# Optimization experiments

Measured on AMD Instinct MI355X. Metric: run time of the kernel, lower is better.

Reference implementation:

```python
import jax, jax.numpy as jnp
import numpy as np

NS, NV, NB, L = 64, 32, 8, 4      # scalar channels, vector channels, bessel bases, layers
EMB = 32                           # atom-type embedding dim
MAX_R = 3.0                        # cutoff radius
NUM_NEIGH = 32.0                   # avg degree used for scatter normalization
N, E = 10000, 320000
NW = NS * 2 + NV * 2               # per-edge tensor-product weights from radial MLP
MAX_TYPES = 10


def smooth_cutoff(x):
    # e3nn md-example smooth_cutoff: 1 for x<0.5, 0 for x>1, cosine blend between
    u = 2.0 * (x - 1.0)
    y = (1.0 - jnp.cos(jnp.pi * u)) * 0.5
    y = jnp.where(u > 0.0, 0.0, y)
    y = jnp.where(u < -1.0, 1.0, y)
    return y


def bessel_basis(r):
    # soft_one_hot_linspace(basis='bessel', cutoff=False) * sqrt(NB)
    n = jnp.arange(1, NB + 1, dtype=r.dtype)
    y = jnp.sqrt(2.0 / MAX_R) * jnp.sin(n * jnp.pi * r[:, None] / MAX_R) / r[:, None]
    return y * np.sqrt(NB).astype(np.float32)


def edge_info(x, src, dst):
    feats, attrs = [], []
    for i in range(2):  # nvec = x.shape[-1] // 3 = 2
        vec = x[src, 3 * i:3 * i + 3] - x[dst, 3 * i:3 * i + 3]  # [E,3]
        r = jnp.linalg.norm(vec, axis=1)
        sh = np.float32(np.sqrt(3.0)) * vec / r[:, None]          # 1x1o SH, component norm
        feats.append(bessel_basis(r))
        attrs.append(smooth_cutoff(r / MAX_R)[:, None] * sh)
    return jnp.concatenate(feats, axis=-1), jnp.stack(attrs, axis=1)  # [E,2*NB], [E,2,3]


def _forward(x, emb_table, W_up, W_proj, fc1, b1, fc2, W_sv, W_vs, W_sc_s, W_sc_v, Ws, Wv, h, mix, node_attr, edge_src, edge_dst):
    n = x.shape[0]
    inv_nb = np.float32(1.0 / np.sqrt(NUM_NEIGH))
    # uplift: 2 input vectors -> NV hidden vectors, NS hidden scalars (zero init)
    xv = x.reshape(n, 2, 3)
    v = jnp.einsum('nic,iv->nvc', xv, W_up)        # [n,NV,3]
    s = jnp.zeros((n, NS), x.dtype)                # [n,NS]
    s_old, v_old = s, v
    attr_emb = emb_table[node_attr]                # [n,EMB]
    xcur = x
    for i in range(L):
        f, a = edge_info(xcur, edge_src, edge_dst)            # [E,2NB], [E,2,3]
        w = jax.nn.silu(f @ fc1[i] + b1[i]) @ fc2[i]          # [E,NW] radial TP weights
        w1 = w[:, :NS * 2].reshape(-1, NS, 2)                 # 0e x 1o -> 1o path weights
        w2 = w[:, NS * 2:].reshape(-1, NV, 2)                 # 1o x 1o -> 0e path weights
        # equivariant tensor-product messages (gather at edge_src)
        t = s[edge_src][:, :, None] * w1                      # [E,NS,2]
        q = jnp.einsum('euv,uvm->evm', t, W_sv[i])            # [E,2,NV]
        msg_v = jnp.einsum('evm,evc->emc', q, a)              # [E,NV,3]
        d = jnp.einsum('euc,evc->euv', v[edge_src], a)        # [E,NV,2]
        msg_s = jnp.einsum('euv,uvm->em', d * w2, W_vs[i])    # [E,NS+NV]
        # scatter-add at edge_dst, normalized by sqrt(num_neighbors)
        agg_s = jnp.zeros((n, NS + NV), x.dtype).at[edge_dst].add(msg_s) * inv_nb
        agg_v = jnp.zeros((n, NV, 3), x.dtype).at[edge_dst].add(msg_v) * inv_nb
        # self-connection: fully-connected TP with node-attr scalars
        sc_s = jnp.einsum('nu,ne,uem->nm', s, attr_emb, W_sc_s[i])
        sc_v = jnp.einsum('nuc,ne,uev->nvc', v, attr_emb, W_sc_v[i])
        cs = sc_s + agg_s
        cv = sc_v + agg_v
        # Gate: silu on scalars, sigmoid gate scalars modulate vectors
        gs = jax.nn.silu(cs[:, :NS])
        gate = jax.nn.sigmoid(cs[:, NS:])
        gv = cv * gate[:, :, None]
        # self-interaction (equivariant linear per degree)
        si_s = s @ Ws[i]
        si_v = jnp.einsum('nuc,uv->nvc', v, Wv[i])
        # verlet-like update
        hi2 = h[i] ** 2
        s_new = 2.0 * s - s_old + hi2 * (mix[i] * gs + (mix[i] - 1.0) * si_s)
        v_new = 2.0 * v - v_old + hi2 * (mix[i] * gv + (mix[i] - 1.0) * si_v)
        s_old, v_old = s, v
        s, v = s_new, v_new
        # project back to x for next layer's edge features
        xcur = jnp.einsum('nvc,vi->nic', v, W_proj).reshape(n, 6)
    return xcur


def setup_inputs() -> dict:
    key = jax.random.key(0)
    ks = jax.random.split(key, 20)
    x = jax.random.normal(ks[0], (N, 6), jnp.float32)
    node_attr = jax.random.randint(ks[1], (N,), 0, MAX_TYPES)
    edge_src = jax.random.randint(ks[2], (E,), 0, N)
    off = jax.random.randint(ks[3], (E,), 1, N)
    edge_dst = (edge_src + off) % N  # no self-loops -> no zero edge_vec
    batch = jnp.zeros((N,), jnp.int32)
    rn = lambda k, sh, sc: jax.random.normal(k, sh, jnp.float32) * np.float32(sc)
    emb_table = rn(ks[4], (MAX_TYPES, EMB), 0.5)
    W_up = rn(ks[5], (2, NV), 1.0 / np.sqrt(2))
    W_proj = rn(ks[6], (NV, 2), 1.0 / np.sqrt(NV))
    fc1 = rn(ks[7], (L, 2 * NB, 64), 1.0 / np.sqrt(2 * NB))
    b1 = jnp.zeros((L, 64), jnp.float32)
    fc2 = rn(ks[8], (L, 64, NW), 1.0 / np.sqrt(64))
    W_sv = rn(ks[9], (L, NS, 2, NV), 1.0 / np.sqrt(NS * 2))
    W_vs = rn(ks[10], (L, NV, 2, NS + NV), 1.0 / np.sqrt(NV * 2))
    W_sc_s = rn(ks[11], (L, NS, EMB, NS + NV), 1.0 / np.sqrt(NS * EMB))
    W_sc_v = rn(ks[12], (L, NV, EMB, NV), 1.0 / np.sqrt(NV * EMB))
    Ws = rn(ks[13], (L, NS, NS), 1.0 / np.sqrt(NS))
    Wv = rn(ks[14], (L, NV, NV), 1.0 / np.sqrt(NV))
    h = jnp.ones((L,), jnp.float32) * 0.01
    mix = jnp.ones((L,), jnp.float32) * 0.5
    return {"x": x, "emb_table": emb_table, "W_up": W_up, "W_proj": W_proj, "fc1": fc1, "b1": b1, "fc2": fc2, "W_sv": W_sv, "W_vs": W_vs, "W_sc_s": W_sc_s, "W_sc_v": W_sc_v, "Ws": Ws, "Wv": Wv, "h": h, "mix": mix, "node_attr": node_attr, "edge_src": edge_src, "edge_dst": edge_dst, "batch": batch}


def reference(x, emb_table, W_up, W_proj, fc1, b1, fc2, W_sv, W_vs, W_sc_s, W_sc_v, Ws, Wv, h, mix, node_attr, edge_src, edge_dst, batch):
    return _forward(x, emb_table, W_up, W_proj, fc1, b1, fc2, W_sv, W_vs, W_sc_s, W_sc_v, Ws, Wv, h, mix, node_attr, edge_src, edge_dst)
```

## Files before the change

kernel.cpp:

```cpp
#include <hip/hip_runtime.h>
#include <math.h>

constexpr int cNS = 64, cNV = 32, cNB = 8, cL = 4, cEMB = 32, cNT = 10;
constexpr float PI_F = 3.14159265358979323846f;
constexpr float INV_SQRT_NN = 0.17677669529663687f;
constexpr float BESSEL_C = 2.3094010767585034f;
constexpr float SQRT3 = 1.7320508075688772f;

typedef unsigned short u16;
typedef unsigned int u32;
typedef __attribute__((ext_vector_type(8))) short bf16x8;
typedef __attribute__((ext_vector_type(4))) float f32x4;
typedef __attribute__((ext_vector_type(2))) float f32x2;
typedef __attribute__((ext_vector_type(4))) int i32x4;

__device__ __forceinline__ u16 f2b(float x) {
  u32 u = __float_as_uint(x);
  return (u16)((u + 0x7fffu + ((u >> 16) & 1u)) >> 16);
}
__device__ __forceinline__ float b2f(u16 h) { return __uint_as_float(((u32)h) << 16); }

__device__ __forceinline__ f32x4 mfma16(bf16x8 a, bf16x8 b, f32x4 c) {
  return __builtin_amdgcn_mfma_f32_16x16x32_bf16(a, b, c, 0, 0, 0);
}


__global__ void k_precompA(const float* __restrict__ emb, const float* __restrict__ Wss,
                           float* __restrict__ A) {
  int idx = blockIdx.x * 256 + threadIdx.x;
  if (idx >= cL * cNT * 64 * 96) return;
  int m = idx % 96;
  int u = (idx / 96) % 64;
  int t = (idx / (96 * 64)) % cNT;
  int l = idx / (96 * 64 * cNT);
  float acc = 0.f;
#pragma unroll
  for (int e = 0; e < 32; ++e)
    acc += emb[t * 32 + e] * Wss[((size_t)(l * 64 + u) * 32 + e) * 96 + m];
  A[idx] = acc;
}

__global__ void k_precompB(const float* __restrict__ emb, const float* __restrict__ Wsv_,
                           float* __restrict__ B) {
  int idx = blockIdx.x * 256 + threadIdx.x;
  if (idx >= cL * cNT * 32 * 32) return;
  int vo = idx % 32;
  int u = (idx / 32) % 32;
  int t = (idx / 1024) % cNT;
  int l = idx / (1024 * cNT);
  float acc = 0.f;
#pragma unroll
  for (int e = 0; e < 32; ++e)
    acc += emb[t * 32 + e] * Wsv_[((size_t)(l * 32 + u) * 32 + e) * 32 + vo];
  B[idx] = acc;
}

__global__ void k_packB(const float* __restrict__ fc2, const float* __restrict__ Wsv,
                        const float* __restrict__ Wvs, const float* __restrict__ fc1,
                        u16* __restrict__ fc2L, u16* __restrict__ WsvL,
                        u16* __restrict__ WvsL, u16* __restrict__ fc1L) {
  int idx = blockIdx.x * 256 + threadIdx.x;
  const int T1 = cL * 12288, T2 = cL * 2 * 2048, T3 = cL * 2 * 3072, T4 = cL * 2048;
  if (idx < T1) {
    int l = idx / 12288, r = idx % 12288;
    int ki = r & 7, tt = r >> 3;
    int nn = tt % 192, kq = tt / 192;
    fc2L[idx] = f2b(fc2[((size_t)(l * 64) + kq * 8 + ki) * 192 + nn]);
  } else if (idx < T1 + T2) {
    int r0 = idx - T1;
    int l = r0 / 4096, r1 = r0 % 4096;
    int k2 = r1 / 2048, r = r1 % 2048;
    int ki = r & 7, tt = r >> 3;
    int mm = tt % 32, kq = tt / 32;
    WsvL[r0] = f2b(Wsv[((size_t)((l * 64 + kq * 8 + ki) * 2) + k2) * 32 + mm]);
  } else if (idx < T1 + T2 + T3) {
    int r0 = idx - T1 - T2;
    int l = r0 / 6144, r1 = r0 % 6144;
    int k2 = r1 / 3072, r = r1 % 3072;
    int ki = r & 7, tt = r >> 3;
    int mm = tt % 96, kq = tt / 96;
    WvsL[r0] = f2b(Wvs[((size_t)((l * 32 + kq * 8 + ki) * 2) + k2) * 96 + mm]);
  } else if (idx < T1 + T2 + T3 + T4) {
    int r0 = idx - T1 - T2 - T3;
    int l = r0 / 2048, r1 = r0 % 2048;
    int kq = r1 / 512, rem = r1 % 512;
    int n = rem / 8, ki = rem & 7;
    fc1L[r0] = (kq < 2) ? f2b(fc1[l * 1024 + (kq * 8 + ki) * 64 + n]) : (u16)0;
  }
}

__global__ void k_init(const float* __restrict__ x, const float* __restrict__ Wup,
                       float* __restrict__ v, float* __restrict__ v_old,
                       float* __restrict__ xcur, int N) {
  int idx = blockIdx.x * 256 + threadIdx.x;
  if (idx >= N * 32) return;
  int n = idx >> 5, vc = idx & 31;
  float w0 = Wup[vc], w1 = Wup[32 + vc];
#pragma unroll
  for (int c = 0; c < 3; ++c) {
    float val = x[n * 6 + c] * w0 + x[n * 6 + 3 + c] * w1;
    v[idx * 3 + c] = val;
    v_old[idx * 3 + c] = val;
  }
  if (vc < 6) xcur[n * 6 + vc] = x[n * 6 + vc];
}


__global__ void k_zero_i(int* __restrict__ p, int n) {
  int i = blockIdx.x * 256 + threadIdx.x;
  if (i < n) p[i] = 0;
}

__global__ void k_hist(const int* __restrict__ edst, int* __restrict__ deg, int E) {
  int e = blockIdx.x * 256 + threadIdx.x;
  if (e < E) atomicAdd(&deg[edst[e]], 1);
}

__global__ __launch_bounds__(1024) void k_scan(const int* __restrict__ deg,
                                               int* __restrict__ row_ptr,
                                               int* __restrict__ cursor, int N) {
  __shared__ int part[1024];
  int t = threadIdx.x;
  int chunk = (N + 1023) / 1024;
  int base = t * chunk;
  int sum = 0;
  for (int i = 0; i < chunk; ++i) {
    int idx = base + i;
    if (idx < N) sum += deg[idx];
  }
  part[t] = sum;
  __syncthreads();
  for (int off = 1; off < 1024; off <<= 1) {
    int val = (t >= off) ? part[t - off] : 0;
    __syncthreads();
    part[t] += val;
    __syncthreads();
  }
  int run = (t > 0) ? part[t - 1] : 0;
  for (int i = 0; i < chunk; ++i) {
    int idx = base + i;
    if (idx < N) {
      row_ptr[idx] = run;
      cursor[idx] = run;
      run += deg[idx];
    }
  }
  if (t == 1023) row_ptr[N] = part[1023];
}

__global__ void k_scatter(const int* __restrict__ esrc, const int* __restrict__ edst,
                          int* __restrict__ cursor, int* __restrict__ esrc_s,
                          int* __restrict__ edst_s, int E) {
  int e = blockIdx.x * 256 + threadIdx.x;
  if (e < E) {
    int d = edst[e];
    int p = atomicAdd(&cursor[d], 1);
    esrc_s[p] = esrc[e];
    edst_s[p] = d;
  }
}

template <bool SZERO>
__global__ __launch_bounds__(256) void k_edge_mfma(
    const float* __restrict__ xcur, const float* __restrict__ s, const float* __restrict__ v,
    const int* __restrict__ esrc_s, const int* __restrict__ edst_s,
    const u16* __restrict__ fc1L, const float* __restrict__ b1,
    const u16* __restrict__ fc2L, const u16* __restrict__ WsvL0,
    const u16* __restrict__ WsvL1, const u16* __restrict__ WvsL0,
    const u16* __restrict__ WvsL1, u16* __restrict__ msgbuf, int E) {
  __shared__ u16 wbAll[4][16 * 200];
  __shared__ float aAll[4][16][6];
  int wid = threadIdx.x >> 6, lane = threadIdx.x & 63;
  int e0 = (blockIdx.x * 4 + wid) * 16;
  if (e0 >= E) return;
  u16* wb = wbAll[wid];
  int lrow = lane & 15, lg = lane >> 4;

  {
    int el = lane >> 2, qq = lane & 3;
    int ge = e0 + el;
    if (ge >= E) ge = E - 1;
    int gs = esrc_s[ge], gd = edst_s[ge];
    float xs[6], xd[6];
    {
      const float2* ps = (const float2*)(xcur + (size_t)gs * 6);
      const float2* pd = (const float2*)(xcur + (size_t)gd * 6);
      float2 A0 = ps[0], A1 = ps[1], A2 = ps[2];
      float2 B0 = pd[0], B1 = pd[1], B2 = pd[2];
      xs[0] = A0.x; xs[1] = A0.y; xs[2] = A1.x; xs[3] = A1.y; xs[4] = A2.x; xs[5] = A2.y;
      xd[0] = B0.x; xd[1] = B0.y; xd[2] = B1.x; xd[3] = B1.y; xd[4] = B2.x; xd[5] = B2.y;
    }
    float f[16], av[6];
#pragma unroll
    for (int i = 0; i < 2; ++i) {
      float vx = xs[3 * i + 0] - xd[3 * i + 0];
      float vy = xs[3 * i + 1] - xd[3 * i + 1];
      float vz = xs[3 * i + 2] - xd[3 * i + 2];
      float r2 = vx * vx + vy * vy + vz * vz;
      float rr = sqrtf(r2);
      float invr = 1.0f / rr;
      float th = (PI_F / 3.0f) * rr;
      float s1, c1;
      __sincosf(th, &s1, &c1);
      float twc = 2.0f * c1;
      float snm = 0.f, sn = s1;
      float fc = BESSEL_C * invr;
#pragma unroll
      for (int nn = 0; nn < 8; ++nn) {
        f[8 * i + nn] = fc * sn;
        float nx = twc * sn - snm;
        snm = sn;
        sn = nx;
      }
      float uu = (2.0f / 3.0f) * rr - 2.0f;
      float cut;
      if (uu > 0.f) cut = 0.f;
      else if (uu < -1.f) cut = 1.f;
      else cut = (1.0f - __cosf(PI_F * uu)) * 0.5f;
      float sc = cut * SQRT3 * invr;
      av[3 * i + 0] = vx * sc; av[3 * i + 1] = vy * sc; av[3 * i + 2] = vz * sc;
    }
    if (qq == 0) {
      u32* fp = (u32*)(wb + 1600 + el * 32);
#pragma unroll
      for (int i = 0; i < 8; ++i)
        fp[i] = (u32)f2b(f[2 * i]) | ((u32)f2b(f[2 * i + 1]) << 16);
#pragma unroll
      for (int i = 8; i < 16; ++i) fp[i] = 0u;
      float* ap = aAll[wid][el];
#pragma unroll
      for (int i = 0; i < 6; ++i) ap[i] = av[i];
    }
  }
  asm volatile("s_waitcnt lgkmcnt(0)" ::: "memory");
  __builtin_amdgcn_sched_barrier(0);

  {
    bf16x8 fA = *(const bf16x8*)(wb + 1600 + lrow * 32 + lg * 8);
    f32x4 hp[4];
#pragma unroll
    for (int nb = 0; nb < 4; ++nb) {
      bf16x8 bB = *(const bf16x8*)(fc1L + (size_t)(lg * 64 + nb * 16 + lrow) * 8);
      f32x4 z = {0.f, 0.f, 0.f, 0.f};
      hp[nb] = mfma16(fA, bB, z);
    }
#pragma unroll
    for (int nb = 0; nb < 4; ++nb) {
      float bias = b1[nb * 16 + lrow];
#pragma unroll
      for (int r = 0; r < 4; ++r) {
        float xv = hp[nb][r] + bias;
        float hv = xv * (1.0f / (1.0f + __expf(-xv)));
        wb[(4 * lg + r) * 72 + nb * 16 + lrow] = f2b(hv);
      }
    }
  }
  asm volatile("s_waitcnt lgkmcnt(0)" ::: "memory");
  __builtin_amdgcn_sched_barrier(0);

  int prow = e0 + lrow;
  if (prow >= E) prow = E - 1;

  bf16x8 ha = *(const bf16x8*)(wb + lrow * 72 + lg * 8);
  bf16x8 hbf = *(const bf16x8*)(wb + lrow * 72 + 32 + lg * 8);
  asm volatile("s_waitcnt lgkmcnt(0)" ::: "memory");

#pragma unroll
  for (int nb = (SZERO ? 8 : 0); nb < 12; ++nb) {
    bf16x8 b0 = *(const bf16x8*)(fc2L + (size_t)(lg * 192 + nb * 16 + lrow) * 8);
    bf16x8 b1v = *(const bf16x8*)(fc2L + (size_t)((4 + lg) * 192 + nb * 16 + lrow) * 8);
    f32x4 c = {0.f, 0.f, 0.f, 0.f};
    c = mfma16(ha, b0, c);
    c = mfma16(hbf, b1v, c);
    int n = nb * 16 + lrow;
    int pn = (n < 128) ? ((n & 1) * 64 + (n >> 1)) : (128 + (n & 1) * 32 + ((n - 128) >> 1));
    int rbase = 4 * lg * 200 + pn;
    wb[rbase] = f2b(c[0]);
    wb[rbase + 200] = f2b(c[1]);
    wb[rbase + 400] = f2b(c[2]);
    wb[rbase + 600] = f2b(c[3]);
  }
  asm volatile("s_waitcnt lgkmcnt(0)" ::: "memory");

  int src = esrc_s[prow];
  const u16* wrow = wb + lrow * 200;

  f32x4 q0[2], q1[2];
  if (!SZERO) {
    const float* sp = s + (size_t)src * 64;
    float sv0[8], sv1[8];
    *(f32x4*)(sv0) = *(const f32x4*)(sp + lg * 8);
    *(f32x4*)(sv0 + 4) = *(const f32x4*)(sp + lg * 8 + 4);
    *(f32x4*)(sv1) = *(const f32x4*)(sp + 32 + lg * 8);
    *(f32x4*)(sv1 + 4) = *(const f32x4*)(sp + 32 + lg * 8 + 4);
    bf16x8 w0a = *(const bf16x8*)(wrow + lg * 8);
    bf16x8 w0b = *(const bf16x8*)(wrow + 32 + lg * 8);
    bf16x8 w1a = *(const bf16x8*)(wrow + 64 + lg * 8);
    bf16x8 w1b = *(const bf16x8*)(wrow + 96 + lg * 8);
    bf16x8 t0a, t0b, t1a, t1b;
#pragma unroll
    for (int j = 0; j < 8; ++j) {
      t0a[j] = (short)f2b(sv0[j] * b2f((u16)w0a[j]));
      t0b[j] = (short)f2b(sv1[j] * b2f((u16)w0b[j]));
      t1a[j] = (short)f2b(sv0[j] * b2f((u16)w1a[j]));
      t1b[j] = (short)f2b(sv1[j] * b2f((u16)w1b[j]));
    }
#pragma unroll
    for (int nb = 0; nb < 2; ++nb) {
      bf16x8 bA = *(const bf16x8*)(WsvL0 + (size_t)(lg * 32 + nb * 16 + lrow) * 8);
      bf16x8 bB = *(const bf16x8*)(WsvL0 + (size_t)((4 + lg) * 32 + nb * 16 + lrow) * 8);
      f32x4 c = {0.f, 0.f, 0.f, 0.f};
      c = mfma16(t0a, bA, c);
      c = mfma16(t0b, bB, c);
      q0[nb] = c;
      bf16x8 bC = *(const bf16x8*)(WsvL1 + (size_t)(lg * 32 + nb * 16 + lrow) * 8);
      bf16x8 bD = *(const bf16x8*)(WsvL1 + (size_t)((4 + lg) * 32 + nb * 16 + lrow) * 8);
      f32x4 c2 = {0.f, 0.f, 0.f, 0.f};
      c2 = mfma16(t1a, bC, c2);
      c2 = mfma16(t1b, bD, c2);
      q1[nb] = c2;
    }
  }

  float a00, a01, a02, a10, a11, a12;
  {
    const float* ap = aAll[wid][lrow];
    a00 = ap[0]; a01 = ap[1]; a02 = ap[2]; a10 = ap[3]; a11 = ap[4]; a12 = ap[5];
  }
  float vl[24];
  {
    const float* vp = v + (size_t)src * 96 + lg * 24;
#pragma unroll
    for (int i = 0; i < 6; ++i) *(f32x4*)(vl + 4 * i) = *(const f32x4*)(vp + 4 * i);
  }
  bf16x8 w2a = *(const bf16x8*)(wrow + 128 + lg * 8);
  bf16x8 w2b = *(const bf16x8*)(wrow + 160 + lg * 8);
  bf16x8 ga, gb;
#pragma unroll
  for (int j = 0; j < 8; ++j) {
    float vx = vl[3 * j], vy = vl[3 * j + 1], vz = vl[3 * j + 2];
    float d0 = vx * a00 + vy * a01 + vz * a02;
    float d1 = vx * a10 + vy * a11 + vz * a12;
    ga[j] = (short)f2b(d0 * b2f((u16)w2a[j]));
    gb[j] = (short)f2b(d1 * b2f((u16)w2b[j]));
  }
  f32x4 mS[6];
#pragma unroll
  for (int nb = 0; nb < 6; ++nb) {
    bf16x8 b0 = *(const bf16x8*)(WvsL0 + (size_t)(lg * 96 + nb * 16 + lrow) * 8);
    bf16x8 b1v = *(const bf16x8*)(WvsL1 + (size_t)(lg * 96 + nb * 16 + lrow) * 8);
    f32x4 c = {0.f, 0.f, 0.f, 0.f};
    c = mfma16(ga, b0, c);
    c = mfma16(gb, b1v, c);
    mS[nb] = c;
  }

  asm volatile("s_waitcnt lgkmcnt(0)" ::: "memory");
#pragma unroll
  for (int nb = 0; nb < 6; ++nb) {
#pragma unroll
    for (int r = 0; r < 4; ++r)
      wb[(4 * lg + r) * 200 + nb * 16 + lrow] = f2b(mS[nb][r]);
  }
  if (!SZERO) {
#pragma unroll
    for (int nb = 0; nb < 2; ++nb) {
#pragma unroll
      for (int r = 0; r < 4; ++r) {
        int el = 4 * lg + r;
        const float* ap = aAll[wid][el];
        float Q0v = q0[nb][r], Q1v = q1[nb][r];
#pragma unroll
        for (int c = 0; c < 3; ++c)
          wb[el * 200 + 96 + c * 32 + nb * 16 + lrow] = f2b(Q0v * ap[c] + Q1v * ap[3 + c]);
      }
    }
  }
  asm volatile("s_waitcnt lgkmcnt(0)" ::: "memory");

  int orow = lane >> 2, oq = lane & 3;
  if (e0 + orow < E) {
    u16* gdst = msgbuf + (size_t)(e0 + orow) * 192;
    const int NIT = SZERO ? 3 : 6;
#pragma unroll
    for (int it = 0; it < NIT; ++it) {
      int col = oq * 8 + it * 32;
      i32x4 d = *(const i32x4*)(wb + orow * 200 + col);
      *(i32x4*)(gdst + col) = d;
    }
  }
}

template <bool SZERO>
__global__ __launch_bounds__(128) void k_gnode(
    const u16* __restrict__ msg, const int* __restrict__ row_ptr,
    float* __restrict__ s, float* __restrict__ sold, float* __restrict__ v,
    float* __restrict__ vold,
    const float* __restrict__ Amat, const float* __restrict__ Bmat,
    const float* __restrict__ Ws, const float* __restrict__ Wv,
    const float* __restrict__ Wproj, const int* __restrict__ nattr,
    const float* __restrict__ hArr, const float* __restrict__ mixArr, int layer,
    float* __restrict__ xout, int N) {
  int n = blockIdx.x;
  int t = threadIdx.x;
  __shared__ float agg[192];
  __shared__ float srow[64];
  __shared__ float vrow[96];
  __shared__ float gateS[32];
  __shared__ float vnewS[96];
  int start = row_ptr[n], end = row_ptr[n + 1];
  int nacc = SZERO ? 48 : 96;
  if (t < nacc) {
    const u16* mp = msg + (size_t)t * 2;
    float l0 = 0.f, h0 = 0.f, l1 = 0.f, h1 = 0.f;
    float l2 = 0.f, h2 = 0.f, l3 = 0.f, h3 = 0.f;
    int p = start;
    for (; p + 4 <= end; p += 4) {
      u32 w0 = *(const u32*)(mp + (size_t)p * 192);
      u32 w1 = *(const u32*)(mp + (size_t)(p + 1) * 192);
      u32 w2 = *(const u32*)(mp + (size_t)(p + 2) * 192);
      u32 w3 = *(const u32*)(mp + (size_t)(p + 3) * 192);
      l0 += b2f((u16)w0); h0 += b2f((u16)(w0 >> 16));
      l1 += b2f((u16)w1); h1 += b2f((u16)(w1 >> 16));
      l2 += b2f((u16)w2); h2 += b2f((u16)(w2 >> 16));
      l3 += b2f((u16)w3); h3 += b2f((u16)(w3 >> 16));
    }
    for (; p < end; ++p) {
      u32 w = *(const u32*)(mp + (size_t)p * 192);
      l0 += b2f((u16)w); h0 += b2f((u16)(w >> 16));
    }
    agg[2 * t] = (l0 + l1 + l2 + l3) * INV_SQRT_NN;
    agg[2 * t + 1] = (h0 + h1 + h2 + h3) * INV_SQRT_NN;
  }
  if (SZERO && t >= 48 && t < 96) {
    agg[2 * t] = 0.f;
    agg[2 * t + 1] = 0.f;
  }
  if (t < 64) srow[t] = s[(size_t)n * 64 + t];
  if (t < 96) vrow[t] = v[(size_t)n * 96 + t];
  __syncthreads();
  int type = nattr[n];
  float hv = hArr[layer];
  float h2v = hv * hv;
  float mx = mixArr[layer];
  float cs = 0.f;
  if (t < 96) {
    cs = agg[t];
    const float* Ac = Amat + (size_t)type * 64 * 96 + t;
#pragma unroll 8
    for (int u = 0; u < 64; ++u) cs += srow[u] * Ac[u * 96];
  }
  if (t >= 64 && t < 96) gateS[t - 64] = 1.0f / (1.0f + __expf(-cs));
  __syncthreads();
  if (t < 64) {
    float gs = cs * (1.0f / (1.0f + __expf(-cs)));
    float sis = 0.f;
#pragma unroll 8
    for (int u = 0; u < 64; ++u) sis += srow[u] * Ws[u * 64 + t];
    float scur = srow[t];
    float sprev = sold[(size_t)n * 64 + t];
    float snew = 2.f * scur - sprev + h2v * (mx * gs + (mx - 1.f) * sis);
    sold[(size_t)n * 64 + t] = scur;
    s[(size_t)n * 64 + t] = snew;
  }
  if (t < 96) {
    int vch = t / 3, c = t - vch * 3;
    float cv = agg[96 + c * 32 + vch];
    const float* Bc = Bmat + (size_t)type * 1024 + vch;
    float scv = 0.f, siv = 0.f;
#pragma unroll 8
    for (int u = 0; u < 32; ++u) {
      float vu = vrow[u * 3 + c];
      scv += vu * Bc[u * 32];
      siv += vu * Wv[u * 32 + vch];
    }
    cv += scv;
    float gv = cv * gateS[vch];
    float vcur = vrow[t];
    float vprev = vold[(size_t)n * 96 + t];
    float vnew = 2.f * vcur - vprev + h2v * (mx * gv + (mx - 1.f) * siv);
    vold[(size_t)n * 96 + t] = vcur;
    v[(size_t)n * 96 + t] = vnew;
    vnewS[t] = vnew;
  }
  __syncthreads();
  if (t < 6) {
    int i = t / 3, c = t - i * 3;
    float acc = 0.f;
#pragma unroll
    for (int vo = 0; vo < 32; ++vo) acc += vnewS[vo * 3 + c] * Wproj[vo * 2 + i];
    xout[(size_t)n * 6 + t] = acc;
  }
}

extern "C" void kernel_launch(void* const* d_in, const int* in_sizes, int n_in,
                              void* d_out, int out_size, void* d_ws, size_t ws_size,
                              hipStream_t stream) {
  const float* x = (const float*)d_in[0];
  const float* emb = (const float*)d_in[1];
  const float* Wup = (const float*)d_in[2];
  const float* Wproj = (const float*)d_in[3];
  const float* fc1 = (const float*)d_in[4];
  const float* b1 = (const float*)d_in[5];
  const float* fc2 = (const float*)d_in[6];
  const float* Wsv = (const float*)d_in[7];
  const float* Wvs = (const float*)d_in[8];
  const float* Wscs = (const float*)d_in[9];
  const float* Wscv = (const float*)d_in[10];
  const float* Ws = (const float*)d_in[11];
  const float* Wv = (const float*)d_in[12];
  const float* hArr = (const float*)d_in[13];
  const float* mixArr = (const float*)d_in[14];
  const int* nattr = (const int*)d_in[15];
  const int* esrc = (const int*)d_in[16];
  const int* edst = (const int*)d_in[17];

  const int N = in_sizes[0] / 6;
  const int E = in_sizes[16];

  float* ws = (float*)d_ws;
  size_t off = 0;
  auto alloc = [&](size_t nf) {
    float* p = ws + off;
    off += (nf + 3) & ~(size_t)3;
    return p;
  };
  float* sbuf = alloc((size_t)N * 64);
  float* sold = alloc((size_t)N * 64);
  float* vbuf = alloc((size_t)N * 96);
  float* vold = alloc((size_t)N * 96);
  float* xcur = alloc((size_t)N * 6);
  float* Amat = alloc((size_t)cL * cNT * 64 * 96);
  float* Bmat = alloc((size_t)cL * cNT * 32 * 32);
  u16* fc2L = (u16*)alloc((size_t)cL * 6144);
  u16* WsvL = (u16*)alloc((size_t)cL * 2048);
  u16* WvsL = (u16*)alloc((size_t)cL * 3072);
  u16* fc1L = (u16*)alloc((size_t)cL * 1024);
  int* deg = (int*)alloc((size_t)(N + 4));
  int* row_ptr = (int*)alloc((size_t)(N + 4));
  int* cursor = (int*)alloc((size_t)(N + 4));
  int* esrc_s = (int*)alloc((size_t)E);
  int* edst_s = (int*)alloc((size_t)E);
  u16* msgbuf = (u16*)alloc((size_t)E * 96);

  hipMemsetAsync(sbuf, 0, sizeof(float) * (size_t)N * 128, stream);
  k_init<<<(N * 32 + 255) / 256, 256, 0, stream>>>(x, Wup, vbuf, vold, xcur, N);
  k_precompA<<<(cL * cNT * 64 * 96 + 255) / 256, 256, 0, stream>>>(emb, Wscs, Amat);
  k_precompB<<<(cL * cNT * 32 * 32 + 255) / 256, 256, 0, stream>>>(emb, Wscv, Bmat);
  {
    int tot = cL * 12288 + cL * 4096 + cL * 6144 + cL * 2048;
    k_packB<<<(tot + 255) / 256, 256, 0, stream>>>(fc2, Wsv, Wvs, fc1, fc2L, WsvL, WvsL, fc1L);
  }
  k_zero_i<<<(N + 255) / 256, 256, 0, stream>>>(deg, N);
  k_hist<<<(E + 255) / 256, 256, 0, stream>>>(edst, deg, E);
  k_scan<<<1, 1024, 0, stream>>>(deg, row_ptr, cursor, N);
  k_scatter<<<(E + 255) / 256, 256, 0, stream>>>(esrc, edst, cursor, esrc_s, edst_s, E);

  int eblocks = ((E + 15) / 16 + 3) / 4;
  for (int l = 0; l < cL; ++l) {
    if (l == 0)
      k_edge_mfma<true><<<eblocks, 256, 0, stream>>>(
          xcur, sbuf, vbuf, esrc_s, edst_s, fc1L + l * 2048, b1 + l * 64,
          fc2L + l * 12288, WsvL + l * 4096, WsvL + l * 4096 + 2048,
          WvsL + l * 6144, WvsL + l * 6144 + 3072, msgbuf, E);
    else
      k_edge_mfma<false><<<eblocks, 256, 0, stream>>>(
          xcur, sbuf, vbuf, esrc_s, edst_s, fc1L + l * 2048, b1 + l * 64,
          fc2L + l * 12288, WsvL + l * 4096, WsvL + l * 4096 + 2048,
          WvsL + l * 6144, WvsL + l * 6144 + 3072, msgbuf, E);
    float* xout = (l == cL - 1) ? (float*)d_out : xcur;
    if (l == 0)
      k_gnode<true><<<N, 128, 0, stream>>>(
          msgbuf, row_ptr, sbuf, sold, vbuf, vold, Amat + (size_t)l * cNT * 64 * 96,
          Bmat + (size_t)l * cNT * 1024, Ws + l * 4096, Wv + l * 1024, Wproj, nattr,
          hArr, mixArr, l, xout, N);
    else
      k_gnode<false><<<N, 128, 0, stream>>>(
          msgbuf, row_ptr, sbuf, sold, vbuf, vold, Amat + (size_t)l * cNT * 64 * 96,
          Bmat + (size_t)l * cNT * 1024, Ws + l * 4096, Wv + l * 1024, Wproj, nattr,
          hArr, mixArr, l, xout, N);
  }
}
```

Measured before the change: 558.0 us.

## Pack bf16 conversions with v_cvt_pk and compact message stride for zero-scalar layer

```diff
diff --git a/kernel.cpp b/kernel.cpp
--- a/kernel.cpp
+++ b/kernel.cpp
@@ -19,6 +19,16 @@
   return (u16)((u + 0x7fffu + ((u >> 16) & 1u)) >> 16);
 }
 __device__ __forceinline__ float b2f(u16 h) { return __uint_as_float(((u32)h) << 16); }
+__device__ __forceinline__ float blo(u32 w) { return __uint_as_float(w << 16); }
+__device__ __forceinline__ float bhi(u32 w) { return __uint_as_float(w & 0xffff0000u); }
+
+__device__ __forceinline__ u32 pkbf(float lo, float hi) {
+  u32 r;
+  asm("v_cvt_pk_bf16_f32 %0, %1, %2" : "=v"(r) : "v"(lo), "v"(hi));
+  return r;
+}
+
+union U8 { bf16x8 v; u32 w[4]; };
 
 __device__ __forceinline__ f32x4 mfma16(bf16x8 a, bf16x8 b, f32x4 c) {
   return __builtin_amdgcn_mfma_f32_16x16x32_bf16(a, b, c, 0, 0, 0);
@@ -223,8 +233,7 @@
     if (qq == 0) {
       u32* fp = (u32*)(wb + 1600 + el * 32);
 #pragma unroll
-      for (int i = 0; i < 8; ++i)
-        fp[i] = (u32)f2b(f[2 * i]) | ((u32)f2b(f[2 * i + 1]) << 16);
+      for (int i = 0; i < 8; ++i) fp[i] = pkbf(f[2 * i], f[2 * i + 1]);
 #pragma unroll
       for (int i = 8; i < 16; ++i) fp[i] = 0u;
       float* ap = aAll[wid][el];
@@ -247,12 +256,19 @@
 #pragma unroll
     for (int nb = 0; nb < 4; ++nb) {
       float bias = b1[nb * 16 + lrow];
+      float hv[4];
 #pragma unroll
       for (int r = 0; r < 4; ++r) {
         float xv = hp[nb][r] + bias;
-        float hv = xv * (1.0f / (1.0f + __expf(-xv)));
-        wb[(4 * lg + r) * 72 + nb * 16 + lrow] = f2b(hv);
+        hv[r] = xv * (1.0f / (1.0f + __expf(-xv)));
       }
+      u32 p01 = pkbf(hv[0], hv[1]);
+      u32 p23 = pkbf(hv[2], hv[3]);
+      int col = nb * 16 + lrow;
+      wb[(4 * lg + 0) * 72 + col] = (u16)p01;
+      wb[(4 * lg + 1) * 72 + col] = (u16)(p01 >> 16);
+      wb[(4 * lg + 2) * 72 + col] = (u16)p23;
+      wb[(4 * lg + 3) * 72 + col] = (u16)(p23 >> 16);
     }
   }
   asm volatile("s_waitcnt lgkmcnt(0)" ::: "memory");
@@ -275,10 +291,12 @@
     int n = nb * 16 + lrow;
     int pn = (n < 128) ? ((n & 1) * 64 + (n >> 1)) : (128 + (n & 1) * 32 + ((n - 128) >> 1));
     int rbase = 4 * lg * 200 + pn;
-    wb[rbase] = f2b(c[0]);
-    wb[rbase + 200] = f2b(c[1]);
-    wb[rbase + 400] = f2b(c[2]);
-    wb[rbase + 600] = f2b(c[3]);
+    u32 p01 = pkbf(c[0], c[1]);
+    u32 p23 = pkbf(c[2], c[3]);
+    wb[rbase] = (u16)p01;
+    wb[rbase + 200] = (u16)(p01 >> 16);
+    wb[rbase + 400] = (u16)p23;
+    wb[rbase + 600] = (u16)(p23 >> 16);
   }
   asm volatile("s_waitcnt lgkmcnt(0)" ::: "memory");
 
@@ -293,31 +311,32 @@
     *(f32x4*)(sv0 + 4) = *(const f32x4*)(sp + lg * 8 + 4);
     *(f32x4*)(sv1) = *(const f32x4*)(sp + 32 + lg * 8);
     *(f32x4*)(sv1 + 4) = *(const f32x4*)(sp + 32 + lg * 8 + 4);
-    bf16x8 w0a = *(const bf16x8*)(wrow + lg * 8);
-    bf16x8 w0b = *(const bf16x8*)(wrow + 32 + lg * 8);
-    bf16x8 w1a = *(const bf16x8*)(wrow + 64 + lg * 8);
-    bf16x8 w1b = *(const bf16x8*)(wrow + 96 + lg * 8);
-    bf16x8 t0a, t0b, t1a, t1b;
-#pragma unroll
-    for (int j = 0; j < 8; ++j) {
-      t0a[j] = (short)f2b(sv0[j] * b2f((u16)w0a[j]));
-      t0b[j] = (short)f2b(sv1[j] * b2f((u16)w0b[j]));
-      t1a[j] = (short)f2b(sv0[j] * b2f((u16)w1a[j]));
-      t1b[j] = (short)f2b(sv1[j] * b2f((u16)w1b[j]));
+    i32x4 W0a = *(const i32x4*)(wrow + lg * 8);
+    i32x4 W0b = *(const i32x4*)(wrow + 32 + lg * 8);
+    i32x4 W1a = *(const i32x4*)(wrow + 64 + lg * 8);
+    i32x4 W1b = *(const i32x4*)(wrow + 96 + lg * 8);
+    U8 t0a, t0b, t1a, t1b;
+#pragma unroll
+    for (int j2 = 0; j2 < 4; ++j2) {
+      u32 wa = (u32)W0a[j2], wbv = (u32)W0b[j2], wc = (u32)W1a[j2], wd = (u32)W1b[j2];
+      t0a.w[j2] = pkbf(sv0[2 * j2] * blo(wa), sv0[2 * j2 + 1] * bhi(wa));
+      t0b.w[j2] = pkbf(sv1[2 * j2] * blo(wbv), sv1[2 * j2 + 1] * bhi(wbv));
+      t1a.w[j2] = pkbf(sv0[2 * j2] * blo(wc), sv0[2 * j2 + 1] * bhi(wc));
+      t1b.w[j2] = pkbf(sv1[2 * j2] * blo(wd), sv1[2 * j2 + 1] * bhi(wd));
     }
 #pragma unroll
     for (int nb = 0; nb < 2; ++nb) {
       bf16x8 bA = *(const bf16x8*)(WsvL0 + (size_t)(lg * 32 + nb * 16 + lrow) * 8);
       bf16x8 bB = *(const bf16x8*)(WsvL0 + (size_t)((4 + lg) * 32 + nb * 16 + lrow) * 8);
       f32x4 c = {0.f, 0.f, 0.f, 0.f};
-      c = mfma16(t0a, bA, c);
-      c = mfma16(t0b, bB, c);
+      c = mfma16(t0a.v, bA, c);
+      c = mfma16(t0b.v, bB, c);
       q0[nb] = c;
       bf16x8 bC = *(const bf16x8*)(WsvL1 + (size_t)(lg * 32 + nb * 16 + lrow) * 8);
       bf16x8 bD = *(const bf16x8*)(WsvL1 + (size_t)((4 + lg) * 32 + nb * 16 + lrow) * 8);
       f32x4 c2 = {0.f, 0.f, 0.f, 0.f};
-      c2 = mfma16(t1a, bC, c2);
-      c2 = mfma16(t1b, bD, c2);
+      c2 = mfma16(t1a.v, bC, c2);
+      c2 = mfma16(t1b.v, bD, c2);
       q1[nb] = c2;
     }
   }
@@ -333,16 +352,25 @@
 #pragma unroll
     for (int i = 0; i < 6; ++i) *(f32x4*)(vl + 4 * i) = *(const f32x4*)(vp + 4 * i);
   }
-  bf16x8 w2a = *(const bf16x8*)(wrow + 128 + lg * 8);
-  bf16x8 w2b = *(const bf16x8*)(wrow + 160 + lg * 8);
-  bf16x8 ga, gb;
-#pragma unroll
-  for (int j = 0; j < 8; ++j) {
-    float vx = vl[3 * j], vy = vl[3 * j + 1], vz = vl[3 * j + 2];
-    float d0 = vx * a00 + vy * a01 + vz * a02;
-    float d1 = vx * a10 + vy * a11 + vz * a12;
-    ga[j] = (short)f2b(d0 * b2f((u16)w2a[j]));
-    gb[j] = (short)f2b(d1 * b2f((u16)w2b[j]));
+  i32x4 W2a = *(const i32x4*)(wrow + 128 + lg * 8);
+  i32x4 W2b = *(const i32x4*)(wrow + 160 + lg * 8);
+  U8 ga, gb;
+#pragma unroll
+  for (int j2 = 0; j2 < 4; ++j2) {
+    float d0a, d1a, d0b, d1b;
+    {
+      float vx = vl[6 * j2 + 0], vy = vl[6 * j2 + 1], vz = vl[6 * j2 + 2];
+      d0a = vx * a00 + vy * a01 + vz * a02;
+      d1a = vx * a10 + vy * a11 + vz * a12;
+    }
+    {
+      float vx = vl[6 * j2 + 3], vy = vl[6 * j2 + 4], vz = vl[6 * j2 + 5];
+      d0b = vx * a00 + vy * a01 + vz * a02;
+      d1b = vx * a10 + vy * a11 + vz * a12;
+    }
+    u32 wa = (u32)W2a[j2], wbv = (u32)W2b[j2];
+    ga.w[j2] = pkbf(d0a * blo(wa), d0b * bhi(wa));
+    gb.w[j2] = pkbf(d1a * blo(wbv), d1b * bhi(wbv));
   }
   f32x4 mS[6];
 #pragma unroll
@@ -350,17 +378,21 @@
     bf16x8 b0 = *(const bf16x8*)(WvsL0 + (size_t)(lg * 96 + nb * 16 + lrow) * 8);
     bf16x8 b1v = *(const bf16x8*)(WvsL1 + (size_t)(lg * 96 + nb * 16 + lrow) * 8);
     f32x4 c = {0.f, 0.f, 0.f, 0.f};
-    c = mfma16(ga, b0, c);
-    c = mfma16(gb, b1v, c);
+    c = mfma16(ga.v, b0, c);
+    c = mfma16(gb.v, b1v, c);
     mS[nb] = c;
   }
 
   asm volatile("s_waitcnt lgkmcnt(0)" ::: "memory");
 #pragma unroll
   for (int nb = 0; nb < 6; ++nb) {
-#pragma unroll
-    for (int r = 0; r < 4; ++r)
-      wb[(4 * lg + r) * 200 + nb * 16 + lrow] = f2b(mS[nb][r]);
+    u32 p01 = pkbf(mS[nb][0], mS[nb][1]);
+    u32 p23 = pkbf(mS[nb][2], mS[nb][3]);
+    int col = nb * 16 + lrow;
+    wb[(4 * lg + 0) * 200 + col] = (u16)p01;
+    wb[(4 * lg + 1) * 200 + col] = (u16)(p01 >> 16);
+    wb[(4 * lg + 2) * 200 + col] = (u16)p23;
+    wb[(4 * lg + 3) * 200 + col] = (u16)(p23 >> 16);
   }
   if (!SZERO) {
 #pragma unroll
@@ -370,9 +402,14 @@
         int el = 4 * lg + r;
         const float* ap = aAll[wid][el];
         float Q0v = q0[nb][r], Q1v = q1[nb][r];
-#pragma unroll
-        for (int c = 0; c < 3; ++c)
-          wb[el * 200 + 96 + c * 32 + nb * 16 + lrow] = f2b(Q0v * ap[c] + Q1v * ap[3 + c]);
+        float v0 = Q0v * ap[0] + Q1v * ap[3];
+        float v1 = Q0v * ap[1] + Q1v * ap[4];
+        float v2 = Q0v * ap[2] + Q1v * ap[5];
+        u32 p01 = pkbf(v0, v1);
+        int base = el * 200 + 96 + nb * 16 + lrow;
+        wb[base] = (u16)p01;
+        wb[base + 32] = (u16)(p01 >> 16);
+        wb[base + 64] = f2b(v2);
       }
     }
   }
@@ -380,7 +417,8 @@
 
   int orow = lane >> 2, oq = lane & 3;
   if (e0 + orow < E) {
-    u16* gdst = msgbuf + (size_t)(e0 + orow) * 192;
+    const int OST = SZERO ? 96 : 192;
+    u16* gdst = msgbuf + (size_t)(e0 + orow) * OST;
     const int NIT = SZERO ? 3 : 6;
 #pragma unroll
     for (int it = 0; it < NIT; ++it) {
@@ -409,28 +447,29 @@
   __shared__ float gateS[32];
   __shared__ float vnewS[96];
   int start = row_ptr[n], end = row_ptr[n + 1];
+  const int STRIDE = SZERO ? 96 : 192;
   int nacc = SZERO ? 48 : 96;
   if (t < nacc) {
     const u16* mp = msg + (size_t)t * 2;
-    float l0 = 0.f, h0 = 0.f, l1 = 0.f, h1 = 0.f;
-    float l2 = 0.f, h2 = 0.f, l3 = 0.f, h3 = 0.f;
+    float aL[4] = {0.f, 0.f, 0.f, 0.f}, aH[4] = {0.f, 0.f, 0.f, 0.f};
     int p = start;
-    for (; p + 4 <= end; p += 4) {
-      u32 w0 = *(const u32*)(mp + (size_t)p * 192);
-      u32 w1 = *(const u32*)(mp + (size_t)(p + 1) * 192);
-      u32 w2 = *(const u32*)(mp + (size_t)(p + 2) * 192);
-      u32 w3 = *(const u32*)(mp + (size_t)(p + 3) * 192);
-      l0 += b2f((u16)w0); h0 += b2f((u16)(w0 >> 16));
-      l1 += b2f((u16)w1); h1 += b2f((u16)(w1 >> 16));
-      l2 += b2f((u16)w2); h2 += b2f((u16)(w2 >> 16));
-      l3 += b2f((u16)w3); h3 += b2f((u16)(w3 >> 16));
+    for (; p + 8 <= end; p += 8) {
+      u32 w[8];
+#pragma unroll
+      for (int k = 0; k < 8; ++k) w[k] = *(const u32*)(mp + (size_t)(p + k) * STRIDE);
+#pragma unroll
+      for (int k = 0; k < 8; ++k) {
+        aL[k & 3] += blo(w[k]);
+        aH[k & 3] += bhi(w[k]);
+      }
     }
     for (; p < end; ++p) {
-      u32 w = *(const u32*)(mp + (size_t)p * 192);
-      l0 += b2f((u16)w); h0 += b2f((u16)(w >> 16));
-    }
-    agg[2 * t] = (l0 + l1 + l2 + l3) * INV_SQRT_NN;
-    agg[2 * t + 1] = (h0 + h1 + h2 + h3) * INV_SQRT_NN;
+      u32 w = *(const u32*)(mp + (size_t)p * STRIDE);
+      aL[0] += blo(w);
+      aH[0] += bhi(w);
+    }
+    agg[2 * t] = (aL[0] + aL[1] + aL[2] + aL[3]) * INV_SQRT_NN;
+    agg[2 * t + 1] = (aH[0] + aH[1] + aH[2] + aH[3]) * INV_SQRT_NN;
   }
   if (SZERO && t >= 48 && t < 96) {
     agg[2 * t] = 0.f;
```

After: 540.3 us. 1.03x faster.
